# Kernel optimization log

Measured on AMD Instinct MI355X. Metric: run time of the kernel, lower is better.

The kernel has to match this reference:

```python
import math
import jax, jax.numpy as jnp
import numpy as np

B, S, E, H = 32, 512, 256, 8

def setup_inputs() -> dict:
    key = jax.random.key(0)
    ks = jax.random.split(key, 9)
    q = jax.random.normal(ks[0], (B, S, E), dtype=jnp.float32)
    k = jax.random.normal(ks[1], (B, S, E), dtype=jnp.float32)
    v = jax.random.normal(ks[2], (B, S, E), dtype=jnp.float32)
    padding_mask = (jax.random.uniform(ks[3], (B, S)) < 0.9).astype(jnp.float32)
    # causal additive mask [S, S]: 0 on/below diagonal, -1e9 above
    causal = jnp.tril(jnp.ones((S, S), dtype=bool))
    attn_mask = jnp.where(causal, 0.0, -1e9).astype(jnp.float32)
    sc = 1.0 / math.sqrt(E)
    Wq = jax.random.normal(ks[4], (H, E, E), dtype=jnp.float32) * sc
    Wk = jax.random.normal(ks[5], (H, E, E), dtype=jnp.float32) * sc
    Wv = jax.random.normal(ks[6], (H, E, E), dtype=jnp.float32) * sc
    Wo = jax.random.normal(ks[7], (E, H * E), dtype=jnp.float32) * (1.0 / math.sqrt(H * E))
    bo = jax.random.normal(ks[8], (E,), dtype=jnp.float32) * 0.01
    return {"q": q, "k": k, "v": v, "padding_mask": padding_mask,
            "attn_mask": attn_mask, "Wq": Wq, "Wk": Wk, "Wv": Wv,
            "Wo": Wo, "bo": bo}

def reference(q, k, v, padding_mask, attn_mask, Wq, Wk, Wv, Wo, bo):
    # Per-head full-width projections, batched over heads.
    # torch Linear: y = x @ W^T  ->  'bse,hde->bhsd'
    Q = jnp.einsum('bse,hde->bhsd', q, Wq)                      # [B,H,S,E]
    K = jnp.einsum('bse,hde->bhsd', k, Wk)
    K = K * padding_mask[:, None, :, None]                      # zero padded keys
    V = jnp.einsum('bse,hde->bhsd', v, Wv)
    scores = jnp.einsum('bhqd,bhkd->bhqk', Q, K) / math.sqrt(E)  # [B,H,S,S]
    scores = scores + attn_mask[None, None, :, :]
    attn = jax.nn.softmax(scores, axis=-1)
    out = jnp.einsum('bhqk,bhkd->bhqd', attn, V)                # [B,H,S,E]
    # concat heads along feature dim: [B,S,H*E]
    out = out.transpose(0, 2, 1, 3).reshape(B, S, H * E)
    return out @ Wo.T + bo                                      # [B,S,E]
```

## Files before the change

### kernel.cpp

```cpp
#include <hip/hip_runtime.h>


typedef unsigned short u16;
typedef __attribute__((ext_vector_type(4))) unsigned short u16x4;
typedef __attribute__((ext_vector_type(8))) unsigned short u16x8;
typedef __attribute__((ext_vector_type(8))) __bf16 bf16x8;
typedef __attribute__((ext_vector_type(4))) float f32x4;
typedef __attribute__((ext_vector_type(2))) unsigned int u32x2;

#define DI __device__ __forceinline__

DI u16 cvt(float f) { return __builtin_bit_cast(u16, (__bf16)f); }

DI void gl_lds16(const void* g, void* l) {
  __builtin_amdgcn_global_load_lds((const __attribute__((address_space(1))) unsigned int*)g,
                                   (__attribute__((address_space(3))) unsigned int*)l, 16, 0, 0);
}

DI bf16x8 lds16(const void* base, int byte_off) {
  return __builtin_bit_cast(bf16x8, *(const u16x8*)((const char*)base + byte_off));
}

#define MFMA __builtin_amdgcn_mfma_f32_16x16x32_bf16

__global__ __launch_bounds__(256) void cvt_k(const float* __restrict__ q, const float* __restrict__ k,
                                             const float* __restrict__ v, const float* __restrict__ pm,
                                             const float* __restrict__ Wq, const float* __restrict__ Wk,
                                             const float* __restrict__ Wv, const float* __restrict__ bo,
                                             u16* __restrict__ qb, u16* __restrict__ kb, u16* __restrict__ vb,
                                             u16* __restrict__ wqb, u16* __restrict__ wkb,
                                             u16* __restrict__ wvb, float* __restrict__ outb) {
  const int z = blockIdx.y;
  if (z >= 3 && z <= 5 && blockIdx.x >= 256) return;
  const size_t i0 = ((size_t)blockIdx.x * 256 + threadIdx.x) * 8;
  if (z == 6) {
    const int c = (int)(i0 & 255);
    f32x4 a = {bo[c], bo[c + 1], bo[c + 2], bo[c + 3]};
    f32x4 d = {bo[c + 4], bo[c + 5], bo[c + 6], bo[c + 7]};
    *(f32x4*)(outb + i0) = a;
    *(f32x4*)(outb + i0 + 4) = d;
    return;
  }
  const float* src;
  u16* dst;
  float sc = 1.f;
  switch (z) {
    case 0: src = q;  dst = qb;  sc = 0.0625f; break;
    case 1: src = k;  dst = kb;  break;
    case 2: src = v;  dst = vb;  break;
    case 3: src = Wq; dst = wqb; break;
    case 4: src = Wk; dst = wkb; break;
    default: src = Wv; dst = wvb; break;
  }
  if (z == 1) sc = pm[i0 >> 8];
  f32x4 a = *(const f32x4*)(src + i0);
  f32x4 d = *(const f32x4*)(src + i0 + 4);
  u16x8 o = {cvt(a.x * sc), cvt(a.y * sc), cvt(a.z * sc), cvt(a.w * sc),
             cvt(d.x * sc), cvt(d.y * sc), cvt(d.z * sc), cvt(d.w * sc)};
  *(u16x8*)(dst + i0) = o;
}

__global__ __launch_bounds__(256) void cvt_wo(const float* __restrict__ Wo, u16* __restrict__ wob) {
  const size_t i0 = ((size_t)blockIdx.x * 256 + threadIdx.x) * 8;
  f32x4 a = *(const f32x4*)(Wo + i0);
  f32x4 d = *(const f32x4*)(Wo + i0 + 4);
  u16x8 o = {cvt(a.x), cvt(a.y), cvt(a.z), cvt(a.w), cvt(d.x), cvt(d.y), cvt(d.z), cvt(d.w)};
  *(u16x8*)(wob + i0) = o;
}

template<int MODE>
__global__ __launch_bounds__(256) void gemm_bt(const u16* __restrict__ A,
                                               const u16* __restrict__ B,
                                               void* __restrict__ C) {
  constexpr int SK = (MODE == 2) ? 2048 : 256;
  constexpr int NIT = (MODE == 2) ? 16 : 4;
  __shared__ __attribute__((aligned(16))) u16 As[128 * 64];
  __shared__ __attribute__((aligned(16))) u16 Bs[128 * 64];

  const int tid = threadIdx.x;
  const int w = tid >> 6, l = tid & 63, lg = l >> 4, lc = l & 15;
  const int gm0 = blockIdx.x * 128, gn0 = blockIdx.y * 128;
  const int z = blockIdx.z;

  const u16* Ap;
  const u16* Bp;
  int kbase = 0;
  if constexpr (MODE == 0) {
    Ap = A;
    Bp = B + (size_t)z * 65536;
  } else if constexpr (MODE == 1) {
    Ap = A + (size_t)(z & 7) * 65536;
    Bp = B + (size_t)(z >> 3) * 131072;
  } else {
    Ap = A;
    Bp = B;
    kbase = z * 1024;
  }

  const f32x4 zero = {0.f, 0.f, 0.f, 0.f};
  f32x4 acc[4][4];
#pragma unroll
  for (int i = 0; i < 4; ++i)
#pragma unroll
    for (int j = 0; j < 4; ++j) acc[i][j] = zero;

  const int wm = (w & 1) * 64, wn = (w >> 1) * 64;

  for (int it = 0; it < NIT; ++it) {
    const int k0 = kbase + it * 64;
    __syncthreads();
#pragma unroll
    for (int p = 0; p < 4; ++p) {
      const int r0 = (w * 4 + p) * 8;
      const int row = r0 + (l >> 3);
      const u16* g = Ap + (size_t)(gm0 + row) * SK + k0 + (((l & 7) << 3) ^ ((row & 7) << 3));
      gl_lds16(g, &As[r0 * 64]);
    }
#pragma unroll
    for (int p = 0; p < 4; ++p) {
      const int r0 = (w * 4 + p) * 8;
      const int row = r0 + (l >> 3);
      const u16* g = Bp + (size_t)(gn0 + row) * SK + k0 + (((l & 7) << 3) ^ ((row & 7) << 3));
      gl_lds16(g, &Bs[r0 * 64]);
    }
    __syncthreads();

#pragma unroll
    for (int kc = 0; kc < 2; ++kc) {
      bf16x8 afr[4], bfr[4];
#pragma unroll
      for (int i = 0; i < 4; ++i)
        afr[i] = lds16(As, (wm + 16 * i + lc) * 128 + ((kc * 64 + lg * 16) ^ ((lc & 7) << 4)));
#pragma unroll
      for (int j = 0; j < 4; ++j)
        bfr[j] = lds16(Bs, (wn + 16 * j + lc) * 128 + ((kc * 64 + lg * 16) ^ ((lc & 7) << 4)));
#pragma unroll
      for (int i = 0; i < 4; ++i)
#pragma unroll
        for (int j = 0; j < 4; ++j)
          acc[i][j] = MFMA(afr[i], bfr[j], acc[i][j], 0, 0, 0);
    }
  }

#pragma unroll
  for (int i = 0; i < 4; ++i)
#pragma unroll
    for (int j = 0; j < 4; ++j)
#pragma unroll
      for (int ii = 0; ii < 4; ++ii) {
        const int m = gm0 + wm + i * 16 + lg * 4 + ii;
        const int n = gn0 + wn + j * 16 + lc;
        const float v = acc[i][j][ii];
        if constexpr (MODE == 0) {
          const int b = m >> 9, s = m & 511;
          ((u16*)C)[((size_t)(b * 8 + z) * 512 + s) * 256 + n] = cvt(v);
        } else if constexpr (MODE == 1) {
          ((u16*)C)[((size_t)z * 256 + m) * 512 + n] = cvt(v);
        } else {
          atomicAdd((float*)C + (size_t)m * 256 + n, v);
        }
      }
}

#define STAGE(KT, BUF) do {                                                               \
    _Pragma("unroll") for (int p = 0; p < 4; ++p) {                                       \
      const int r0_ = w * 8 + p * 2;                                                      \
      const int row_ = r0_ + (l >> 5);                                                    \
      const u16* g_ = Kbh + (size_t)((KT) * 64 + row_) * 256 +                            \
                      (((l & 31) << 3) ^ ((row_ & 7) << 3));                              \
      gl_lds16(g_, &Ks[BUF][r0_ * 256]);                                                  \
    }                                                                                     \
    _Pragma("unroll") for (int p = 0; p < 4; ++p) {                                       \
      const int r0_ = w * 32 + p * 8;                                                     \
      const int row_ = r0_ + (l >> 3);                                                    \
      const u16* g_ = Vbh + (size_t)row_ * 512 + (KT) * 64 +                              \
                      (((l & 7) << 3) ^ ((row_ & 7) << 3));                               \
      gl_lds16(g_, &Vs[BUF][r0_ * 64]);                                                   \
    }                                                                                     \
  } while (0)

#define PROCESS() do {                                                                    \
    f32x4 st[4];                                                                          \
    _Pragma("unroll") for (int nf = 0; nf < 4; ++nf) st[nf] = zero;                       \
    _Pragma("unroll") for (int nf = 0; nf < 4; ++nf) {                                    \
      const int ro = (nf * 16 + lc) * 512;                                                \
      _Pragma("unroll") for (int kc = 0; kc < 8; ++kc) {                                  \
        bf16x8 kf = lds16(ksb, ro + ((kc * 64 + lg * 16) ^ ((lc & 7) << 4)));             \
        st[nf] = MFMA(kf, qf[kc], st[nf], 0, 0, 0);                                       \
      }                                                                                   \
    }                                                                                     \
    const int qrow_ = qtv * 128 + w * 16 + lc;                                            \
    float mt_ = -3.0e38f;                                                                 \
    _Pragma("unroll") for (int nf = 0; nf < 4; ++nf)                                      \
      _Pragma("unroll") for (int ii = 0; ii < 4; ++ii) {                                  \
        const int key_ = kt * 64 + nf * 16 + lg * 4 + ii;                                 \
        float s_ = st[nf][ii];                                                            \
        if (key_ > qrow_) s_ = -3.0e38f;                                                  \
        st[nf][ii] = s_;                                                                  \
        mt_ = fmaxf(mt_, s_);                                                             \
      }                                                                                   \
    mt_ = fmaxf(mt_, __shfl_xor(mt_, 16));                                                \
    mt_ = fmaxf(mt_, __shfl_xor(mt_, 32));                                                \
    if (!__all(mt_ - m_run <= 8.f)) {                                   \
      const float mn_ = fmaxf(m_run, mt_);                                                \
      const float sf_ = __expf(m_run - mn_);                                              \
      m_run = mn_;                                                                        \
      l_run *= sf_;                                                                       \
      float sfi_[4];                                                                      \
      _Pragma("unroll") for (int ii = 0; ii < 4; ++ii) sfi_[ii] = __shfl(sf_, lg * 4 + ii); \
      _Pragma("unroll") for (int nn = 0; nn < 16; ++nn)                                   \
        _Pragma("unroll") for (int ii = 0; ii < 4; ++ii) acc[nn][ii] *= sfi_[ii];         \
    }                                                                                     \
    float rs_ = 0.f;                                                                      \
    char* pb_ = (char*)&Ps[w][0];                                                         \
    _Pragma("unroll") for (int nf = 0; nf < 4; ++nf) {                                    \
      u32x2 pr_;                                                                          \
      _Pragma("unroll") for (int c = 0; c < 2; ++c) {                                     \
        const float p0_ = __expf(st[nf][2 * c] - m_run);                                  \
        const float p1_ = __expf(st[nf][2 * c + 1] - m_run);                              \
        rs_ += p0_ + p1_;                                                                 \
        pr_[c] = (unsigned int)cvt(p0_) | ((unsigned int)cvt(p1_) << 16);                 \
      }                                                                                   \
      *(u32x2*)(pb_ + (lc * 128 + ((nf * 32 + lg * 8) ^ ((lc & 7) << 4)))) = pr_;         \
    }                                                                                     \
    rs_ += __shfl_xor(rs_, 16);                                                           \
    rs_ += __shfl_xor(rs_, 32);                                                           \
    l_run += rs_;                                                                         \
    bf16x8 pf_[2];                                                                        \
    _Pragma("unroll") for (int kc = 0; kc < 2; ++kc)                                      \
      pf_[kc] = lds16(pb_, lc * 128 + ((kc * 64 + lg * 16) ^ ((lc & 7) << 4)));           \
    _Pragma("unroll") for (int nn = 0; nn < 16; ++nn) {                                   \
      const int ro = (nn * 16 + lc) * 128;                                                \
      _Pragma("unroll") for (int kc = 0; kc < 2; ++kc) {                                  \
        bf16x8 vf = lds16(vsb, ro + ((kc * 64 + lg * 16) ^ ((lc & 7) << 4)));             \
        acc[nn] = MFMA(pf_[kc], vf, acc[nn], 0, 0, 0);                                    \
      }                                                                                   \
    }                                                                                     \
  } while (0)

#define LOADQ(QT) do {                                                                    \
    const u16* qp_ = Qbh + (size_t)((QT) * 128 + w * 16 + lc) * 256 + lg * 8;             \
    _Pragma("unroll") for (int kc = 0; kc < 8; ++kc)                                      \
      qf[kc] = __builtin_bit_cast(bf16x8, *(const u16x8*)(qp_ + kc * 32));                \
  } while (0)

#define RESETST() do {                                                                    \
    m_run = -3.0e38f; l_run = 0.f;                                                        \
    _Pragma("unroll") for (int nn = 0; nn < 16; ++nn) acc[nn] = zero;                     \
  } while (0)

#define WRITEOUT(QT) do {                                                                 \
    const float inv_ = 1.0f / l_run;                                                      \
    _Pragma("unroll") for (int ii = 0; ii < 4; ++ii) {                                    \
      const float li_ = __shfl(inv_, lg * 4 + ii);                                        \
      const int q_ = (QT) * 128 + w * 16 + lg * 4 + ii;                                   \
      u16* op_ = AO + ((size_t)(b * 512 + q_) * 8 + h) * 256 + lc;                        \
      _Pragma("unroll") for (int nn = 0; nn < 16; ++nn)                                   \
        op_[nn * 16] = cvt(acc[nn][ii] * li_);                                            \
    }                                                                                     \
  } while (0)

__global__ __launch_bounds__(512) void attn_k(const u16* __restrict__ Qb,
                                              const u16* __restrict__ Kb,
                                              const u16* __restrict__ Vt,
                                              u16* __restrict__ AO) {
  __shared__ __attribute__((aligned(16))) u16 Ks[2][64 * 256];
  __shared__ __attribute__((aligned(16))) u16 Vs[2][256 * 64];
  __shared__ __attribute__((aligned(16))) u16 Ps[8][16 * 64];

  const int bx = blockIdx.x;
  const int bh = blockIdx.y;
  const int b = bh >> 3, h = bh & 7;
  const int tid = threadIdx.x;
  const int w = tid >> 6, l = tid & 63, lg = l >> 4, lc = l & 15;

  const int qtA = 3 - bx, qtB = bx;
  const int NA = 2 * (qtA + 1);
  const int NT = NA + 2 * (qtB + 1);

  const u16* Qbh = Qb + (size_t)bh * (512 * 256);
  const u16* Kbh = Kb + (size_t)bh * (512 * 256);
  const u16* Vbh = Vt + (size_t)bh * (256 * 512);

  const f32x4 zero = {0.f, 0.f, 0.f, 0.f};
  bf16x8 qf[8];
  f32x4 acc[16];
  float m_run, l_run;

  LOADQ(qtA);
  RESETST();
  STAGE(0, 0);
  int cur = 0;

  for (int i = 0; i < NT; ++i) {
    __syncthreads();
    if (i == NA) {
      WRITEOUT(qtA);
      LOADQ(qtB);
      RESETST();
    }
    if (i + 1 < NT) {
      const int ktn = (i + 1 < NA) ? i + 1 : i + 1 - NA;
      STAGE(ktn, cur ^ 1);
    }
    const int kt = (i < NA) ? i : i - NA;
    const int qtv = (i < NA) ? qtA : qtB;
    const bool act = (kt * 64 <= qtv * 128 + w * 16 + 15);
    const u16* ksb = &Ks[cur][0];
    const u16* vsb = &Vs[cur][0];
    if (act) { PROCESS(); }
    cur ^= 1;
  }
  WRITEOUT(qtB);
}

extern "C" void kernel_launch(void* const* d_in, const int* in_sizes, int n_in,
                              void* d_out, int out_size, void* d_ws, size_t ws_size,
                              hipStream_t stream) {
  const float* q  = (const float*)d_in[0];
  const float* k  = (const float*)d_in[1];
  const float* v  = (const float*)d_in[2];
  const float* pm = (const float*)d_in[3];
  const float* Wq = (const float*)d_in[5];
  const float* Wk = (const float*)d_in[6];
  const float* Wv = (const float*)d_in[7];
  const float* Wo = (const float*)d_in[8];
  const float* bo = (const float*)d_in[9];

  const size_t NBH = 33554432ull;
  u16* Qb = (u16*)d_ws;
  u16* Kf = Qb + NBH;
  u16* Vt = Kf + NBH;
  u16* X  = Vt + NBH;
  u16* qb = X;
  u16* kb = X + 4194304;
  u16* vb = X + 8388608;
  u16* Wqb = X + 12582912;
  u16* Wkb = Wqb + 524288;
  u16* Wvb = Wkb + 524288;
  u16* AO = X;
  u16* Wob = Qb;

  cvt_k<<<dim3(2048, 7), 256, 0, stream>>>(q, k, v, pm, Wq, Wk, Wv, bo,
                                           qb, kb, vb, Wqb, Wkb, Wvb, (float*)d_out);
  gemm_bt<0><<<dim3(128, 2, 8), 256, 0, stream>>>(qb, Wqb, Qb);
  gemm_bt<0><<<dim3(128, 2, 8), 256, 0, stream>>>(kb, Wkb, Kf);
  gemm_bt<1><<<dim3(2, 4, 256), 256, 0, stream>>>(Wvb, vb, Vt);
  attn_k<<<dim3(2, 256, 1), 512, 0, stream>>>(Qb, Kf, Vt, AO);
  cvt_wo<<<dim3(256, 1), 256, 0, stream>>>(Wo, Wob);
  gemm_bt<2><<<dim3(128, 2, 2), 256, 0, stream>>>(AO, Wob, d_out);
}
```

Baseline: 341.7 us.

## Double-buffer GEMM tiles, merge Q/K projections, skip causal masking, use exp2

The projection GEMM now double-buffers its LDS tiles so the next k-slice loads while MFMAs run on the current one, and the Q and K projections are merged into a single launch via the z dimension. In attention, fully unmasked key tiles skip the per-element causal compare, and softmax uses exp2f with log2(e) folded into the Q prescale. The attention grid is flattened with a remapped block-to-(b,h) order, which may change cache locality. Double buffering doubles GEMM LDS use, which may lower occupancy.

```diff
diff --git a/kernel.cpp b/kernel.cpp
--- a/kernel.cpp
+++ b/kernel.cpp
@@ -45,7 +45,7 @@
   u16* dst;
   float sc = 1.f;
   switch (z) {
-    case 0: src = q;  dst = qb;  sc = 0.0625f; break;
+    case 0: src = q;  dst = qb;  sc = 0.0901684400f; break;
     case 1: src = k;  dst = kb;  break;
     case 2: src = v;  dst = vb;  break;
     case 3: src = Wq; dst = wqb; break;
@@ -68,14 +68,27 @@
   *(u16x8*)(wob + i0) = o;
 }
 
+#define STAGEG(K0, BUF) do {                                                              \
+    _Pragma("unroll") for (int p_ = 0; p_ < 4; ++p_) {                                    \
+      const int r0_ = (w * 4 + p_) * 8;                                                   \
+      const int row_ = r0_ + (l >> 3);                                                    \
+      const u16* ga_ = Ap + (size_t)(gm0 + row_) * SK + (K0) +                            \
+                       (((l & 7) << 3) ^ ((row_ & 7) << 3));                              \
+      gl_lds16(ga_, &As[BUF][r0_ * 64]);                                                  \
+      const u16* gb_ = Bp + (size_t)(gn0 + row_) * SK + (K0) +                            \
+                       (((l & 7) << 3) ^ ((row_ & 7) << 3));                              \
+      gl_lds16(gb_, &Bs[BUF][r0_ * 64]);                                                  \
+    }                                                                                     \
+  } while (0)
+
 template<int MODE>
 __global__ __launch_bounds__(256) void gemm_bt(const u16* __restrict__ A,
                                                const u16* __restrict__ B,
                                                void* __restrict__ C) {
   constexpr int SK = (MODE == 2) ? 2048 : 256;
   constexpr int NIT = (MODE == 2) ? 16 : 4;
-  __shared__ __attribute__((aligned(16))) u16 As[128 * 64];
-  __shared__ __attribute__((aligned(16))) u16 Bs[128 * 64];
+  __shared__ __attribute__((aligned(16))) u16 As[2][128 * 64];
+  __shared__ __attribute__((aligned(16))) u16 Bs[2][128 * 64];
 
   const int tid = threadIdx.x;
   const int w = tid >> 6, l = tid & 63, lg = l >> 4, lc = l & 15;
@@ -86,7 +99,7 @@
   const u16* Bp;
   int kbase = 0;
   if constexpr (MODE == 0) {
-    Ap = A;
+    Ap = A + (size_t)(z >> 3) * 4194304;
     Bp = B + (size_t)z * 65536;
   } else if constexpr (MODE == 1) {
     Ap = A + (size_t)(z & 7) * 65536;
@@ -106,40 +119,29 @@
 
   const int wm = (w & 1) * 64, wn = (w >> 1) * 64;
 
+  STAGEG(kbase, 0);
+  int cur = 0;
+
   for (int it = 0; it < NIT; ++it) {
-    const int k0 = kbase + it * 64;
     __syncthreads();
-#pragma unroll
-    for (int p = 0; p < 4; ++p) {
-      const int r0 = (w * 4 + p) * 8;
-      const int row = r0 + (l >> 3);
-      const u16* g = Ap + (size_t)(gm0 + row) * SK + k0 + (((l & 7) << 3) ^ ((row & 7) << 3));
-      gl_lds16(g, &As[r0 * 64]);
-    }
-#pragma unroll
-    for (int p = 0; p < 4; ++p) {
-      const int r0 = (w * 4 + p) * 8;
-      const int row = r0 + (l >> 3);
-      const u16* g = Bp + (size_t)(gn0 + row) * SK + k0 + (((l & 7) << 3) ^ ((row & 7) << 3));
-      gl_lds16(g, &Bs[r0 * 64]);
-    }
-    __syncthreads();
+    if (it + 1 < NIT) STAGEG(kbase + (it + 1) * 64, cur ^ 1);
 
 #pragma unroll
     for (int kc = 0; kc < 2; ++kc) {
       bf16x8 afr[4], bfr[4];
 #pragma unroll
       for (int i = 0; i < 4; ++i)
-        afr[i] = lds16(As, (wm + 16 * i + lc) * 128 + ((kc * 64 + lg * 16) ^ ((lc & 7) << 4)));
+        afr[i] = lds16(&As[cur][0], (wm + 16 * i + lc) * 128 + ((kc * 64 + lg * 16) ^ ((lc & 7) << 4)));
 #pragma unroll
       for (int j = 0; j < 4; ++j)
-        bfr[j] = lds16(Bs, (wn + 16 * j + lc) * 128 + ((kc * 64 + lg * 16) ^ ((lc & 7) << 4)));
+        bfr[j] = lds16(&Bs[cur][0], (wn + 16 * j + lc) * 128 + ((kc * 64 + lg * 16) ^ ((lc & 7) << 4)));
 #pragma unroll
       for (int i = 0; i < 4; ++i)
 #pragma unroll
         for (int j = 0; j < 4; ++j)
           acc[i][j] = MFMA(afr[i], bfr[j], acc[i][j], 0, 0, 0);
     }
+    cur ^= 1;
   }
 
 #pragma unroll
@@ -153,7 +155,8 @@
         const float v = acc[i][j][ii];
         if constexpr (MODE == 0) {
           const int b = m >> 9, s = m & 511;
-          ((u16*)C)[((size_t)(b * 8 + z) * 512 + s) * 256 + n] = cvt(v);
+          u16* Cq = (u16*)C + (size_t)(z >> 3) * 33554432;
+          Cq[((size_t)(b * 8 + (z & 7)) * 512 + s) * 256 + n] = cvt(v);
         } else if constexpr (MODE == 1) {
           ((u16*)C)[((size_t)z * 256 + m) * 512 + n] = cvt(v);
         } else {
@@ -189,21 +192,26 @@
         st[nf] = MFMA(kf, qf[kc], st[nf], 0, 0, 0);                                       \
       }                                                                                   \
     }                                                                                     \
-    const int qrow_ = qtv * 128 + w * 16 + lc;                                            \
     float mt_ = -3.0e38f;                                                                 \
-    _Pragma("unroll") for (int nf = 0; nf < 4; ++nf)                                      \
-      _Pragma("unroll") for (int ii = 0; ii < 4; ++ii) {                                  \
-        const int key_ = kt * 64 + nf * 16 + lg * 4 + ii;                                 \
-        float s_ = st[nf][ii];                                                            \
-        if (key_ > qrow_) s_ = -3.0e38f;                                                  \
-        st[nf][ii] = s_;                                                                  \
-        mt_ = fmaxf(mt_, s_);                                                             \
-      }                                                                                   \
+    if (kt * 64 + 63 <= qtv * 128 + w * 16) {                   \
+      _Pragma("unroll") for (int nf = 0; nf < 4; ++nf)                                    \
+        _Pragma("unroll") for (int ii = 0; ii < 4; ++ii) mt_ = fmaxf(mt_, st[nf][ii]);    \
+    } else {                                                                              \
+      const int qrow_ = qtv * 128 + w * 16 + lc;                                          \
+      _Pragma("unroll") for (int nf = 0; nf < 4; ++nf)                                    \
+        _Pragma("unroll") for (int ii = 0; ii < 4; ++ii) {                                \
+          const int key_ = kt * 64 + nf * 16 + lg * 4 + ii;                               \
+          float s_ = st[nf][ii];                                                          \
+          if (key_ > qrow_) s_ = -3.0e38f;                                                \
+          st[nf][ii] = s_;                                                                \
+          mt_ = fmaxf(mt_, s_);                                                           \
+        }                                                                                 \
+    }                                                                                     \
     mt_ = fmaxf(mt_, __shfl_xor(mt_, 16));                                                \
     mt_ = fmaxf(mt_, __shfl_xor(mt_, 32));                                                \
     if (!__all(mt_ - m_run <= 8.f)) {                                   \
       const float mn_ = fmaxf(m_run, mt_);                                                \
-      const float sf_ = __expf(m_run - mn_);                                              \
+      const float sf_ = exp2f(m_run - mn_);                                               \
       m_run = mn_;                                                                        \
       l_run *= sf_;                                                                       \
       float sfi_[4];                                                                      \
@@ -216,8 +224,8 @@
     _Pragma("unroll") for (int nf = 0; nf < 4; ++nf) {                                    \
       u32x2 pr_;                                                                          \
       _Pragma("unroll") for (int c = 0; c < 2; ++c) {                                     \
-        const float p0_ = __expf(st[nf][2 * c] - m_run);                                  \
-        const float p1_ = __expf(st[nf][2 * c + 1] - m_run);                              \
+        const float p0_ = exp2f(st[nf][2 * c] - m_run);                                   \
+        const float p1_ = exp2f(st[nf][2 * c + 1] - m_run);                               \
         rs_ += p0_ + p1_;                                                                 \
         pr_[c] = (unsigned int)cvt(p0_) | ((unsigned int)cvt(p1_) << 16);                 \
       }                                                                                   \
@@ -268,8 +276,9 @@
   __shared__ __attribute__((aligned(16))) u16 Vs[2][256 * 64];
   __shared__ __attribute__((aligned(16))) u16 Ps[8][16 * 64];
 
-  const int bx = blockIdx.x;
-  const int bh = blockIdx.y;
+  const int wgid = blockIdx.x;
+  const int bh = (wgid >> 4) * 8 + (wgid & 7);
+  const int bx = (wgid >> 3) & 1;
   const int b = bh >> 3, h = bh & 7;
   const int tid = threadIdx.x;
   const int w = tid >> 6, l = tid & 63, lg = l >> 4, lc = l & 15;
@@ -343,10 +352,9 @@
 
   cvt_k<<<dim3(2048, 7), 256, 0, stream>>>(q, k, v, pm, Wq, Wk, Wv, bo,
                                            qb, kb, vb, Wqb, Wkb, Wvb, (float*)d_out);
-  gemm_bt<0><<<dim3(128, 2, 8), 256, 0, stream>>>(qb, Wqb, Qb);
-  gemm_bt<0><<<dim3(128, 2, 8), 256, 0, stream>>>(kb, Wkb, Kf);
+  gemm_bt<0><<<dim3(128, 2, 16), 256, 0, stream>>>(qb, Wqb, Qb);
   gemm_bt<1><<<dim3(2, 4, 256), 256, 0, stream>>>(Wvb, vb, Vt);
-  attn_k<<<dim3(2, 256, 1), 512, 0, stream>>>(Qb, Kf, Vt, AO);
+  attn_k<<<dim3(512, 1, 1), 512, 0, stream>>>(Qb, Kf, Vt, AO);
   cvt_wo<<<dim3(256, 1), 256, 0, stream>>>(Wo, Wob);
   gemm_bt<2><<<dim3(128, 2, 2), 256, 0, stream>>>(AO, Wob, d_out);
 }
```

Result: faster. 334.8 us (-2.0%).
